# Kernel optimization log

Hardware: AMD Instinct MI355X
Metric: run time of the kernel (lower is better)

Reference implementation:

```python
import jax, jax.numpy as jnp
import numpy as np

N = 50000
E_RAND = 800000
IN0 = 128
HEADS = 4
C = 64  # per-head out channels
HC = HEADS * C  # 256, concat output width
SLOPE = 0.2
DIMS_IN = [IN0, HC, HC]


def _gat_layer(x, src, dst, W, att_src, att_dst, bias):
    # x: [N, F_in]; W: [F_in, H*C]; att_*: [H, C]; bias: [H*C]
    h = (x @ W).reshape(N, HEADS, C)                      # [N,H,C]
    a_src = jnp.einsum('nhc,hc->nh', h, att_src)          # [N,H]
    a_dst = jnp.einsum('nhc,hc->nh', h, att_dst)          # [N,H]
    e = jax.nn.leaky_relu(a_src[src] + a_dst[dst], SLOPE)  # [E,H]
    # segment softmax over incoming edges per destination node
    m = jax.ops.segment_max(e, dst, num_segments=N)       # [N,H]
    m = jnp.where(jnp.isfinite(m), m, 0.0)
    ex = jnp.exp(e - m[dst])                              # [E,H]
    denom = jax.ops.segment_sum(ex, dst, num_segments=N)  # [N,H]
    alpha = ex / (denom[dst] + 1e-16)                     # [E,H]
    msg = h[src] * alpha[:, :, None]                      # [E,H,C]
    out = jax.ops.segment_sum(msg, dst, num_segments=N)   # [N,H,C]
    return out.reshape(N, HC) + bias


def setup_inputs() -> dict:
    key = jax.random.key(0)
    ks = jax.random.split(key, 16)
    x = jax.random.normal(ks[0], (N, IN0), dtype=jnp.float32)
    src = jax.random.randint(ks[1], (E_RAND,), 0, N, dtype=jnp.int32)
    dst = jax.random.randint(ks[2], (E_RAND,), 0, N, dtype=jnp.int32)
    loops = jnp.arange(N, dtype=jnp.int32)  # PyG GATConv adds self-loops
    edge_index = jnp.stack([jnp.concatenate([src, loops]),
                            jnp.concatenate([dst, loops])])  # [2, E_RAND+N]
    inp = {'x': x, 'edge_index': edge_index}
    ki = 3
    for l, f_in in enumerate(DIMS_IN):
        s = 1.0 / np.sqrt(f_in)
        inp[f'W{l}'] = jax.random.uniform(ks[ki], (f_in, HC), jnp.float32, -s, s)
        inp[f'att_src{l}'] = jax.random.uniform(ks[ki + 1], (HEADS, C), jnp.float32, -s, s)
        inp[f'att_dst{l}'] = jax.random.uniform(ks[ki + 2], (HEADS, C), jnp.float32, -s, s)
        inp[f'bias{l}'] = jnp.zeros((HC,), jnp.float32)
        ki += 3
    return inp


def reference(x, edge_index, W0, att_src0, att_dst0, bias0,
              W1, att_src1, att_dst1, bias1,
              W2, att_src2, att_dst2, bias2):
    src, dst = edge_index[0], edge_index[1]
    params = [(W0, att_src0, att_dst0, bias0),
              (W1, att_src1, att_dst1, bias1),
              (W2, att_src2, att_dst2, bias2)]
    for W, a_s, a_d, b in params:
        x = jax.nn.relu(_gat_layer(x, src, dst, W, a_s, a_d, b))
    return x
```

## Files before the change

### kernel.cpp

```cpp
#include <hip/hip_runtime.h>
#include <hip/hip_fp16.h>
#include <math.h>

#define IN0    128
#define HEADS  4
#define CDIM   64
#define HC     256
#define SLOPE  0.2f
#define NPAD   50176
#define BK     32

typedef __attribute__((ext_vector_type(8))) _Float16 f16x8;
typedef __attribute__((ext_vector_type(4))) float f32x4;

__device__ __forceinline__ float h2f(ushort u) {
    __half h = *(const __half*)&u;
    return __half2float(h);
}
__device__ __forceinline__ ushort f2h(float f) {
    __half h = __float2half_rn(f);
    return *(ushort*)&h;
}


__device__ __forceinline__ void wconv_body(const float* __restrict__ W,
                                           ushort* __restrict__ Wc, int K, int b) {
    int tid = b * 256 + threadIdx.x;
    int n = tid & 255;
    int k = tid >> 8;
    if (k >= K) return;
    Wc[(size_t)(k >> 5) * (HC * BK) + n * BK + (k & 31)] = f2h(W[(size_t)k * HC + n]);
}

__global__ __launch_bounds__(256) void k_prep(
        const int* __restrict__ dst_rand, int E_rand, int* __restrict__ deg,
        const float* __restrict__ x0, ushort* __restrict__ Xc, int totalx,
        const float* __restrict__ W0, ushort* __restrict__ Wc0,
        const float* __restrict__ W1, ushort* __restrict__ Wc1,
        const float* __restrict__ W2, ushort* __restrict__ Wc2,
        int B0, int B1) {
    int b = blockIdx.x;
    if (b < B0) {
        int i = b * 256 + threadIdx.x;
        if (i < E_rand) atomicAdd(&deg[dst_rand[i]], 1);
        return;
    }
    b -= B0;
    if (b < B1) {
        int i = b * 256 + threadIdx.x;
        if (i < totalx) {
            int n = i >> 7, k = i & 127;
            Xc[(size_t)(k >> 5) * (NPAD * BK) + n * BK + (k & 31)] = f2h(x0[i]);
        }
        return;
    }
    b -= B1;
    if (b < 128) { wconv_body(W0, Wc0, 128, b); return; }
    b -= 128;
    if (b < 256) { wconv_body(W1, Wc1, 256, b); return; }
    b -= 256;
    wconv_body(W2, Wc2, 256, b);
}


__global__ __launch_bounds__(1024) void k_scan(const int* __restrict__ deg, int Nn,
                                               int* __restrict__ rowptr,
                                               int* __restrict__ cur) {
    __shared__ int smem[1024];
    int tid = threadIdx.x;
    int pre = 0;
    int limit = blockIdx.x * 1024;
    for (int i = tid; i < limit; i += 1024) pre += deg[i];
    smem[tid] = pre;
    __syncthreads();
    #pragma unroll
    for (int d = 512; d >= 1; d >>= 1) {
        if (tid < d) smem[tid] += smem[tid + d];
        __syncthreads();
    }
    int s_off = smem[0];
    __syncthreads();
    int i = blockIdx.x * 1024 + tid;
    int v = (i < Nn) ? deg[i] : 0;
    smem[tid] = v;
    __syncthreads();
    #pragma unroll
    for (int d = 1; d < 1024; d <<= 1) {
        int t = 0;
        if (tid >= d) t = smem[tid - d];
        __syncthreads();
        smem[tid] += t;
        __syncthreads();
    }
    if (i < Nn) {
        int e = s_off + smem[tid] - v;
        rowptr[i] = e;
        cur[i] = e;
    }
    if (blockIdx.x == gridDim.x - 1 && tid == 1023) rowptr[Nn] = s_off + smem[1023];
}

__global__ void k_scatter(const int* __restrict__ src, const int* __restrict__ dst, int E_rand,
                          int* __restrict__ cur, int* __restrict__ csr_src) {
    int i = blockIdx.x * blockDim.x + threadIdx.x;
    if (i < E_rand) {
        int d = dst[i];
        int p = atomicAdd(&cur[d], 1);
        csr_src[p] = src[i];
    }
}


template<int K>
__global__ __launch_bounds__(256) void k_gemm_att(const ushort* __restrict__ Xc,
                                                  const ushort* __restrict__ Wc,
                                                  const float* __restrict__ attS,
                                                  const float* __restrict__ attD,
                                                  ushort* __restrict__ H16out,
                                                  float* __restrict__ a_src_v,
                                                  float* __restrict__ a_dst_v,
                                                  int M) {
    int id    = blockIdx.x;
    int group = id >> 4;
    int sub   = id & 15;
    int row0  = (group * 8 + (sub & 7)) * 128;
    int colb  = sub >> 3;
    int col0  = colb * 128;

    int t    = threadIdx.x;
    int wave = t >> 6, lane = t & 63;
    int wm = wave & 1, wn = wave >> 1;
    int quad = lane >> 4, l16 = lane & 15;

    f32x4 acc[4][4];
    #pragma unroll
    for (int i = 0; i < 4; i++)
        #pragma unroll
        for (int j = 0; j < 4; j++) acc[i][j] = (f32x4){0.f, 0.f, 0.f, 0.f};

    constexpr int NK = K / BK;
    #pragma unroll
    for (int kc = 0; kc < NK; kc++) {
        f16x8 a[4], b[4];
        #pragma unroll
        for (int mt = 0; mt < 4; mt++) {
            size_t ga = (size_t)kc * (NPAD * BK)
                      + (size_t)(row0 + wm * 64 + mt * 16 + l16) * BK + quad * 8;
            a[mt] = *(const f16x8*)&Xc[ga];
        }
        #pragma unroll
        for (int nt = 0; nt < 4; nt++) {
            size_t gb = (size_t)kc * (HC * BK)
                      + (size_t)(col0 + wn * 64 + nt * 16 + l16) * BK + quad * 8;
            b[nt] = *(const f16x8*)&Wc[gb];
        }
        #pragma unroll
        for (int mt = 0; mt < 4; mt++)
            #pragma unroll
            for (int nt = 0; nt < 4; nt++)
                acc[mt][nt] = __builtin_amdgcn_mfma_f32_16x16x32_f16(a[mt], b[nt], acc[mt][nt], 0, 0, 0);
    }

    #pragma unroll
    for (int mt = 0; mt < 4; mt++) {
        #pragma unroll
        for (int r = 0; r < 4; r++) {
            int row = row0 + wm*64 + mt*16 + quad*4 + r;
            if (row >= M) continue;
            #pragma unroll
            for (int nt = 0; nt < 4; nt++) {
                size_t idx = (size_t)row * HC + col0 + wn*64 + nt*16 + l16;
                H16out[idx] = f2h(acc[mt][nt][r]);
            }
        }
    }

    int headw = colb * 2 + wn;
    float sS[4], sD[4];
    #pragma unroll
    for (int nt = 0; nt < 4; nt++) {
        sS[nt] = attS[headw * CDIM + nt*16 + l16];
        sD[nt] = attD[headw * CDIM + nt*16 + l16];
    }
    #pragma unroll
    for (int mt = 0; mt < 4; mt++) {
        #pragma unroll
        for (int r = 0; r < 4; r++) {
            float ps = 0.f, pd = 0.f;
            #pragma unroll
            for (int nt = 0; nt < 4; nt++) {
                float av = acc[mt][nt][r];
                ps += av * sS[nt];
                pd += av * sD[nt];
            }
            #pragma unroll
            for (int d = 1; d <= 8; d <<= 1) {
                ps += __shfl_xor(ps, d);
                pd += __shfl_xor(pd, d);
            }
            int row = row0 + wm*64 + mt*16 + quad*4 + r;
            if (l16 == 0 && row < M) {
                a_src_v[row * HEADS + headw] = ps;
                a_dst_v[row * HEADS + headw] = pd;
            }
        }
    }
}


__global__ __launch_bounds__(256) void k_aggregate(
        const ushort* __restrict__ H16,
        const float* __restrict__ a_src_v,
        const float* __restrict__ a_dst_v,
        const int* __restrict__ rowptr, const int* __restrict__ csr_src,
        const float* __restrict__ bias,
        float* __restrict__ out_f32,
        ushort* __restrict__ out_h16c,
        int Nn) {
    int wave  = threadIdx.x >> 6;
    int lane  = threadIdx.x & 63;
    int slice = blockIdx.x & 1;
    int n = (blockIdx.x >> 1) * 4 + wave;
    if (n >= Nn) return;

    int e32 = lane >> 1;
    int hs2 = lane & 1;
    int hgl = slice * 2 + hs2;
    int e2  = lane >> 5;
    int ha2 = (lane >> 4) & 1;
    int c4  = (lane & 15) * 4;
    int chS = ha2 * CDIM + c4;

    int beg = rowptr[n], end = rowptr[n + 1];
    int deg = end - beg;
    float adst_s = a_dst_v[n * HEADS + hgl];
    float es = a_src_v[n * HEADS + hgl] + adst_s;
    es = fmaxf(es, SLOPE * es);
    float ex_self_s = __expf(es);

    float ssum = 0.f;
    float4 acc = make_float4(0.f, 0.f, 0.f, 0.f);
    const char* Hb = (const char*)H16 + (size_t)(slice * 128 + chS) * 2;

    for (int base = 0; base < deg; base += 32) {
        int cnt = min(32, deg - base);
        int s_l = 0; float ex_l = 0.f;
        if (e32 < cnt) {
            s_l = csr_src[beg + base + e32];
            float e = a_src_v[s_l * HEADS + hgl] + adst_s;
            e = fmaxf(e, SLOPE * e);
            ex_l = __expf(e);
            ssum += ex_l;
        }
        int off_l = s_l * (HC * 2);
        int cnt4 = (cnt + 3) & ~3;
        for (int j = 0; j < cnt4; j += 4) {
            int sl0 = ((j + e2) << 1) | ha2;
            int sl1 = ((j + 2 + e2) << 1) | ha2;
            float a0 = __shfl(ex_l,  sl0);
            int   o0 = __shfl(off_l, sl0);
            float a1 = __shfl(ex_l,  sl1);
            int   o1 = __shfl(off_l, sl1);
            ushort4 u0 = *(const ushort4*)(Hb + o0);
            ushort4 u1 = *(const ushort4*)(Hb + o1);
            acc.x += a0 * h2f(u0.x); acc.y += a0 * h2f(u0.y);
            acc.z += a0 * h2f(u0.z); acc.w += a0 * h2f(u0.w);
            acc.x += a1 * h2f(u1.x); acc.y += a1 * h2f(u1.y);
            acc.z += a1 * h2f(u1.z); acc.w += a1 * h2f(u1.w);
        }
    }
    #pragma unroll
    for (int d = 2; d <= 32; d <<= 1) ssum += __shfl_xor(ssum, d);
    ssum += ex_self_s;
    acc.x += __shfl_xor(acc.x, 32);
    acc.y += __shfl_xor(acc.y, 32);
    acc.z += __shfl_xor(acc.z, 32);
    acc.w += __shfl_xor(acc.w, 32);
    float den_a = __shfl(ssum, ha2);
    float exs_a = __shfl(ex_self_s, ha2);

    ushort4 us = *(const ushort4*)((const char*)H16 + (size_t)n * (HC * 2)
                                   + (size_t)(slice * 128 + chS) * 2);
    float rden = 1.f / (den_a + 1e-16f);
    int ch = slice * 128 + chS;
    float4 b = *(const float4*)&bias[ch];
    float4 o;
    o.x = fmaxf((acc.x + exs_a * h2f(us.x)) * rden + b.x, 0.f);
    o.y = fmaxf((acc.y + exs_a * h2f(us.y)) * rden + b.y, 0.f);
    o.z = fmaxf((acc.z + exs_a * h2f(us.z)) * rden + b.z, 0.f);
    o.w = fmaxf((acc.w + exs_a * h2f(us.w)) * rden + b.w, 0.f);

    if (e2 == 0) {
        if (out_f32) {
            *(float4*)&out_f32[(size_t)n * HC + ch] = o;
        }
        if (out_h16c) {
            size_t idx = (size_t)(ch >> 5) * (NPAD * BK) + (size_t)n * BK + (ch & 31);
            *(ushort4*)&out_h16c[idx] = make_ushort4(f2h(o.x), f2h(o.y), f2h(o.z), f2h(o.w));
        }
    }
}


extern "C" void kernel_launch(void* const* d_in, const int* in_sizes, int n_in,
                              void* d_out, int out_size, void* d_ws, size_t ws_size,
                              hipStream_t stream) {
    const float* x0   = (const float*)d_in[0];
    const int*   eidx = (const int*)d_in[1];
    int Nn = in_sizes[0] / IN0;
    int E  = in_sizes[1] / 2;
    int E_rand = E - Nn;
    const int* srcp = eidx;
    const int* dstp = eidx + E;

    const float* Wl[3]    = {(const float*)d_in[2],  (const float*)d_in[6],  (const float*)d_in[10]};
    const float* attS[3]  = {(const float*)d_in[3],  (const float*)d_in[7],  (const float*)d_in[11]};
    const float* attD[3]  = {(const float*)d_in[4],  (const float*)d_in[8],  (const float*)d_in[12]};
    const float* biasl[3] = {(const float*)d_in[5],  (const float*)d_in[9],  (const float*)d_in[13]};
    int Kdims[3] = {IN0, HC, HC};

    char* p = (char*)d_ws;
    ushort* h16    = (ushort*)p; p += (size_t)NPAD * HC * sizeof(ushort);
    ushort* Xc     = (ushort*)p; p += (size_t)NPAD * HC * sizeof(ushort);
    float*  a_src_v= (float*)p;  p += (size_t)Nn * HEADS * sizeof(float);
    float*  a_dst_v= (float*)p;  p += (size_t)Nn * HEADS * sizeof(float);
    int*    rowptr = (int*)p;    p += (size_t)(Nn + 1) * sizeof(int);
    int*    deg    = (int*)p;    p += (size_t)Nn * sizeof(int);
    int*    cur    = (int*)p;    p += (size_t)Nn * sizeof(int);
    int*    csr_src= (int*)p;    p += (size_t)E_rand * sizeof(int);
    ushort* Wc[3];
    for (int l = 0; l < 3; l++) {
        Wc[l] = (ushort*)p; p += (size_t)HC * Kdims[l] * sizeof(ushort);
    }

    int NB = (Nn + 1023) / 1024;
    int B0 = (E_rand + 255) / 256;
    int B1 = (Nn * IN0 + 255) / 256;
    int Bprep = B0 + B1 + 128 + 256 + 256;

    hipMemsetAsync(deg, 0, (size_t)Nn * sizeof(int), stream);
    k_prep<<<Bprep, 256, 0, stream>>>(dstp, E_rand, deg,
                                      x0, Xc, Nn * IN0,
                                      Wl[0], Wc[0], Wl[1], Wc[1], Wl[2], Wc[2],
                                      B0, B1);
    k_scan<<<NB, 1024, 0, stream>>>(deg, Nn, rowptr, cur);
    k_scatter<<<(E_rand + 255) / 256, 256, 0, stream>>>(srcp, dstp, E_rand, cur, csr_src);

    dim3 g(784);
    dim3 ga(2 * ((Nn + 3) / 4));
    for (int l = 0; l < 3; l++) {
        if (l == 0)
            k_gemm_att<128><<<g, 256, 0, stream>>>(Xc, Wc[l], attS[l], attD[l],
                                                   h16, a_src_v, a_dst_v, Nn);
        else
            k_gemm_att<256><<<g, 256, 0, stream>>>(Xc, Wc[l], attS[l], attD[l],
                                                   h16, a_src_v, a_dst_v, Nn);
        if (l < 2) {
            k_aggregate<<<ga, 256, 0, stream>>>(h16, a_src_v, a_dst_v, rowptr, csr_src,
                                                biasl[l], nullptr, Xc, Nn);
        } else {
            k_aggregate<<<ga, 256, 0, stream>>>(h16, a_src_v, a_dst_v, rowptr, csr_src,
                                                biasl[l], (float*)d_out, nullptr, Nn);
        }
    }
}
```

Measured before the change: 394.2 us.

## Precompute per-edge attention weights in a separate edge-parallel kernel

Adds a CSR destination array and a new edge-parallel kernel that computes the exponentiated leaky-relu attention score for all four heads of each edge and stores them head-major. The aggregation kernel then streams these precomputed weights and source indices directly, dropping the per-chunk exp computation and shuffle broadcast. This trades extra global traffic (writing and reading 4 floats per edge per layer, plus csr_dst) and one extra launch per layer for a simpler, less latency-bound gather loop. Padding on csr_src and wpl allows unmasked reads past the segment end.

```diff
diff --git a/kernel.cpp b/kernel.cpp
--- a/kernel.cpp
+++ b/kernel.cpp
@@ -101,12 +101,14 @@
 }
 
 __global__ void k_scatter(const int* __restrict__ src, const int* __restrict__ dst, int E_rand,
-                          int* __restrict__ cur, int* __restrict__ csr_src) {
+                          int* __restrict__ cur, int* __restrict__ csr_src,
+                          int* __restrict__ csr_dst) {
     int i = blockIdx.x * blockDim.x + threadIdx.x;
     if (i < E_rand) {
         int d = dst[i];
         int p = atomicAdd(&cur[d], 1);
         csr_src[p] = src[i];
+        csr_dst[p] = d;
     }
 }
 
@@ -200,19 +202,39 @@
             }
             int row = row0 + wm*64 + mt*16 + quad*4 + r;
             if (l16 == 0 && row < M) {
-                a_src_v[row * HEADS + headw] = ps;
-                a_dst_v[row * HEADS + headw] = pd;
+                a_src_v[(size_t)row * 4 + headw] = ps;
+                a_dst_v[(size_t)row * 4 + headw] = pd;
             }
         }
     }
+}
+
+
+__global__ __launch_bounds__(256) void k_edgew(
+        const int* __restrict__ csr_src, const int* __restrict__ csr_dst, int E_rand,
+        const float* __restrict__ aI_src, const float* __restrict__ aI_dst,
+        float* __restrict__ wpl, int EPAD) {
+    int p = blockIdx.x * 256 + threadIdx.x;
+    if (p >= E_rand) return;
+    int s = csr_src[p], d = csr_dst[p];
+    float4 as = *(const float4*)&aI_src[(size_t)s * 4];
+    float4 ad = *(const float4*)&aI_dst[(size_t)d * 4];
+    float e0 = as.x + ad.x, e1 = as.y + ad.y, e2 = as.z + ad.z, e3 = as.w + ad.w;
+    e0 = fmaxf(e0, SLOPE * e0); e1 = fmaxf(e1, SLOPE * e1);
+    e2 = fmaxf(e2, SLOPE * e2); e3 = fmaxf(e3, SLOPE * e3);
+    wpl[0 * (size_t)EPAD + p] = __expf(e0);
+    wpl[1 * (size_t)EPAD + p] = __expf(e1);
+    wpl[2 * (size_t)EPAD + p] = __expf(e2);
+    wpl[3 * (size_t)EPAD + p] = __expf(e3);
 }
 
 
 __global__ __launch_bounds__(256) void k_aggregate(
         const ushort* __restrict__ H16,
-        const float* __restrict__ a_src_v,
-        const float* __restrict__ a_dst_v,
+        const float* __restrict__ aI_src,
+        const float* __restrict__ aI_dst,
         const int* __restrict__ rowptr, const int* __restrict__ csr_src,
+        const float* __restrict__ wpl, int EPAD,
         const float* __restrict__ bias,
         float* __restrict__ out_f32,
         ushort* __restrict__ out_h16c,
@@ -223,72 +245,59 @@
     int n = (blockIdx.x >> 1) * 4 + wave;
     if (n >= Nn) return;
 
-    int e32 = lane >> 1;
-    int hs2 = lane & 1;
-    int hgl = slice * 2 + hs2;
     int e2  = lane >> 5;
     int ha2 = (lane >> 4) & 1;
     int c4  = (lane & 15) * 4;
     int chS = ha2 * CDIM + c4;
+    int hgl = slice * 2 + ha2;
 
     int beg = rowptr[n], end = rowptr[n + 1];
     int deg = end - beg;
-    float adst_s = a_dst_v[n * HEADS + hgl];
-    float es = a_src_v[n * HEADS + hgl] + adst_s;
-    es = fmaxf(es, SLOPE * es);
-    float ex_self_s = __expf(es);
-
-    float ssum = 0.f;
+    const float* wh = wpl + (size_t)hgl * EPAD;
+    const char* Hb = (const char*)H16 + (size_t)(slice * 128 + chS) * 2;
+
+    float wsum = 0.f;
     float4 acc = make_float4(0.f, 0.f, 0.f, 0.f);
-    const char* Hb = (const char*)H16 + (size_t)(slice * 128 + chS) * 2;
-
-    for (int base = 0; base < deg; base += 32) {
-        int cnt = min(32, deg - base);
-        int s_l = 0; float ex_l = 0.f;
-        if (e32 < cnt) {
-            s_l = csr_src[beg + base + e32];
-            float e = a_src_v[s_l * HEADS + hgl] + adst_s;
-            e = fmaxf(e, SLOPE * e);
-            ex_l = __expf(e);
-            ssum += ex_l;
-        }
-        int off_l = s_l * (HC * 2);
-        int cnt4 = (cnt + 3) & ~3;
-        for (int j = 0; j < cnt4; j += 4) {
-            int sl0 = ((j + e2) << 1) | ha2;
-            int sl1 = ((j + 2 + e2) << 1) | ha2;
-            float a0 = __shfl(ex_l,  sl0);
-            int   o0 = __shfl(off_l, sl0);
-            float a1 = __shfl(ex_l,  sl1);
-            int   o1 = __shfl(off_l, sl1);
-            ushort4 u0 = *(const ushort4*)(Hb + o0);
-            ushort4 u1 = *(const ushort4*)(Hb + o1);
-            acc.x += a0 * h2f(u0.x); acc.y += a0 * h2f(u0.y);
-            acc.z += a0 * h2f(u0.z); acc.w += a0 * h2f(u0.w);
-            acc.x += a1 * h2f(u1.x); acc.y += a1 * h2f(u1.y);
-            acc.z += a1 * h2f(u1.z); acc.w += a1 * h2f(u1.w);
-        }
-    }
-    #pragma unroll
-    for (int d = 2; d <= 32; d <<= 1) ssum += __shfl_xor(ssum, d);
-    ssum += ex_self_s;
+
+    for (int j = 0; j < deg; j += 4) {
+        int p0 = beg + j + e2;
+        int p1 = p0 + 2;
+        bool m0 = (j + e2)     < deg;
+        bool m1 = (j + e2 + 2) < deg;
+        int s0 = csr_src[p0];
+        int s1 = csr_src[p1];
+        float w0 = wh[p0];
+        float w1 = wh[p1];
+        s0 = m0 ? s0 : 0;  w0 = m0 ? w0 : 0.f;
+        s1 = m1 ? s1 : 0;  w1 = m1 ? w1 : 0.f;
+        ushort4 u0 = *(const ushort4*)(Hb + (size_t)s0 * (HC * 2));
+        ushort4 u1 = *(const ushort4*)(Hb + (size_t)s1 * (HC * 2));
+        wsum += w0 + w1;
+        acc.x += w0 * h2f(u0.x); acc.y += w0 * h2f(u0.y);
+        acc.z += w0 * h2f(u0.z); acc.w += w0 * h2f(u0.w);
+        acc.x += w1 * h2f(u1.x); acc.y += w1 * h2f(u1.y);
+        acc.z += w1 * h2f(u1.z); acc.w += w1 * h2f(u1.w);
+    }
+
+    wsum  += __shfl_xor(wsum, 32);
     acc.x += __shfl_xor(acc.x, 32);
     acc.y += __shfl_xor(acc.y, 32);
     acc.z += __shfl_xor(acc.z, 32);
     acc.w += __shfl_xor(acc.w, 32);
-    float den_a = __shfl(ssum, ha2);
-    float exs_a = __shfl(ex_self_s, ha2);
-
-    ushort4 us = *(const ushort4*)((const char*)H16 + (size_t)n * (HC * 2)
-                                   + (size_t)(slice * 128 + chS) * 2);
-    float rden = 1.f / (den_a + 1e-16f);
+
+    float es = aI_src[(size_t)n * 4 + hgl] + aI_dst[(size_t)n * 4 + hgl];
+    es = fmaxf(es, SLOPE * es);
+    float exs = __expf(es);
+
+    ushort4 us = *(const ushort4*)(Hb + (size_t)n * (HC * 2));
+    float rden = 1.f / (wsum + exs + 1e-16f);
     int ch = slice * 128 + chS;
     float4 b = *(const float4*)&bias[ch];
     float4 o;
-    o.x = fmaxf((acc.x + exs_a * h2f(us.x)) * rden + b.x, 0.f);
-    o.y = fmaxf((acc.y + exs_a * h2f(us.y)) * rden + b.y, 0.f);
-    o.z = fmaxf((acc.z + exs_a * h2f(us.z)) * rden + b.z, 0.f);
-    o.w = fmaxf((acc.w + exs_a * h2f(us.w)) * rden + b.w, 0.f);
+    o.x = fmaxf((acc.x + exs * h2f(us.x)) * rden + b.x, 0.f);
+    o.y = fmaxf((acc.y + exs * h2f(us.y)) * rden + b.y, 0.f);
+    o.z = fmaxf((acc.z + exs * h2f(us.z)) * rden + b.z, 0.f);
+    o.w = fmaxf((acc.w + exs * h2f(us.w)) * rden + b.w, 0.f);
 
     if (e2 == 0) {
         if (out_f32) {
@@ -319,6 +328,8 @@
     const float* biasl[3] = {(const float*)d_in[5],  (const float*)d_in[9],  (const float*)d_in[13]};
     int Kdims[3] = {IN0, HC, HC};
 
+    int EPAD = E_rand + 8;
+
     char* p = (char*)d_ws;
     ushort* h16    = (ushort*)p; p += (size_t)NPAD * HC * sizeof(ushort);
     ushort* Xc     = (ushort*)p; p += (size_t)NPAD * HC * sizeof(ushort);
@@ -327,7 +338,9 @@
     int*    rowptr = (int*)p;    p += (size_t)(Nn + 1) * sizeof(int);
     int*    deg    = (int*)p;    p += (size_t)Nn * sizeof(int);
     int*    cur    = (int*)p;    p += (size_t)Nn * sizeof(int);
-    int*    csr_src= (int*)p;    p += (size_t)E_rand * sizeof(int);
+    int*    csr_src= (int*)p;    p += (size_t)EPAD * sizeof(int);
+    int*    csr_dst= (int*)p;    p += (size_t)E_rand * sizeof(int);
+    float*  wpl    = (float*)p;  p += (size_t)HEADS * EPAD * sizeof(float);
     ushort* Wc[3];
     for (int l = 0; l < 3; l++) {
         Wc[l] = (ushort*)p; p += (size_t)HC * Kdims[l] * sizeof(ushort);
@@ -344,9 +357,11 @@
                                       Wl[0], Wc[0], Wl[1], Wc[1], Wl[2], Wc[2],
                                       B0, B1);
     k_scan<<<NB, 1024, 0, stream>>>(deg, Nn, rowptr, cur);
-    k_scatter<<<(E_rand + 255) / 256, 256, 0, stream>>>(srcp, dstp, E_rand, cur, csr_src);
+    k_scatter<<<(E_rand + 255) / 256, 256, 0, stream>>>(srcp, dstp, E_rand, cur,
+                                                        csr_src, csr_dst);
 
     dim3 g(784);
+    dim3 ge((E_rand + 255) / 256);
     dim3 ga(2 * ((Nn + 3) / 4));
     for (int l = 0; l < 3; l++) {
         if (l == 0)
@@ -355,12 +370,14 @@
         else
             k_gemm_att<256><<<g, 256, 0, stream>>>(Xc, Wc[l], attS[l], attD[l],
                                                    h16, a_src_v, a_dst_v, Nn);
+        k_edgew<<<ge, 256, 0, stream>>>(csr_src, csr_dst, E_rand,
+                                        a_src_v, a_dst_v, wpl, EPAD);
         if (l < 2) {
             k_aggregate<<<ga, 256, 0, stream>>>(h16, a_src_v, a_dst_v, rowptr, csr_src,
-                                                biasl[l], nullptr, Xc, Nn);
+                                                wpl, EPAD, biasl[l], nullptr, Xc, Nn);
         } else {
             k_aggregate<<<ga, 256, 0, stream>>>(h16, a_src_v, a_dst_v, rowptr, csr_src,
-                                                biasl[l], (float*)d_out, nullptr, Nn);
-        }
-    }
-}
+                                                wpl, EPAD, biasl[l], (float*)d_out, nullptr, Nn);
+        }
+    }
+}
```

Result: slower. 430.5 us (+9.2%).
